# Performance work log

Measured on AMD Instinct MI355X. Metric: run time of the kernel, lower is better.

The kernel has to match this reference:

```python
import jax, jax.numpy as jnp
import numpy as np
from jax import lax

NPOINT = 1024
RADIUS = 0.2
NSAMPLE = 32
BN_EPS = 1e-5


def square_distance(src, dst):
    # src: [B,N,3], dst: [B,M,3] -> [B,N,M]
    d = -2.0 * jnp.einsum('bnc,bmc->bnm', src, dst)
    d = d + jnp.sum(src * src, -1)[:, :, None]
    d = d + jnp.sum(dst * dst, -1)[:, None, :]
    return d


def farthest_point_sample(xyz, npoint):
    # Deterministic start at index 0 (torch version uses a random start).
    B, N, _ = xyz.shape
    batch = jnp.arange(B)

    def step(carry, _):
        distance, farthest = carry
        centroid = xyz[batch, farthest][:, None, :]          # [B,1,3]
        dist = jnp.sum((xyz - centroid) ** 2, -1)            # [B,N]
        distance = jnp.minimum(distance, dist)
        new_far = jnp.argmax(distance, -1).astype(jnp.int32)
        return (distance, new_far), farthest

    init = (jnp.full((B, N), 1e10, xyz.dtype), jnp.zeros((B,), jnp.int32))
    _, cents = lax.scan(step, init, None, length=npoint)     # [npoint,B]
    return cents.T                                           # [B,npoint]


def index_points(points, idx):
    # points: [B,N,C], idx: [B,...] -> [B,...,C]
    return jax.vmap(lambda p, i: p[i])(points, idx)


def query_ball_point(radius, nsample, xyz, new_xyz):
    B, N, _ = xyz.shape
    sqr = square_distance(new_xyz, xyz)                      # [B,S,N]
    gidx = jnp.where(sqr > radius * radius, N,
                     jnp.arange(N, dtype=jnp.int32)[None, None, :])
    gidx = jnp.sort(gidx, axis=-1)[:, :, :nsample]           # [B,S,nsample]
    first = gidx[:, :, :1]
    return jnp.where(gidx == N, first, gidx)


def conv_bn_relu(x, w, b, g, beta):
    # x: [B,Cin,K,S]; 1x1 conv + training-mode BN + ReLU
    y = jnp.einsum('bcks,oc->boks', x, w) + b[None, :, None, None]
    mean = jnp.mean(y, axis=(0, 2, 3), keepdims=True)
    var = jnp.var(y, axis=(0, 2, 3), keepdims=True)
    y = (y - mean) * lax.rsqrt(var + BN_EPS)
    y = y * g[None, :, None, None] + beta[None, :, None, None]
    return jax.nn.relu(y)


def setup_inputs() -> dict:
    key = jax.random.key(0)
    ks = jax.random.split(key, 8)
    B, N, D = 16, 4096, 64
    inp = {
        'xyz': jax.random.uniform(ks[0], (B, N, 3), jnp.float32),
        'points': jax.random.normal(ks[1], (B, N, D), jnp.float32),
        'w1': jax.random.normal(ks[2], (64, 67), jnp.float32) * 0.1,
        'b1': jax.random.normal(ks[3], (64,), jnp.float32) * 0.1,
        'g1': jnp.ones((64,), jnp.float32),
        'beta1': jnp.zeros((64,), jnp.float32),
        'w2': jax.random.normal(ks[4], (64, 64), jnp.float32) * 0.1,
        'b2': jax.random.normal(ks[5], (64,), jnp.float32) * 0.1,
        'g2': jnp.ones((64,), jnp.float32),
        'beta2': jnp.zeros((64,), jnp.float32),
        'w3': jax.random.normal(ks[6], (128, 64), jnp.float32) * 0.1,
        'b3': jax.random.normal(ks[7], (128,), jnp.float32) * 0.1,
        'g3': jnp.ones((128,), jnp.float32),
        'beta3': jnp.zeros((128,), jnp.float32),
    }
    return inp


def reference(xyz, points, w1, b1, g1, beta1, w2, b2, g2, beta2, w3, b3, g3, beta3):
    B, N, C = xyz.shape
    fps_idx = farthest_point_sample(xyz, NPOINT)                 # [B,S]
    new_xyz = index_points(xyz, fps_idx)                         # [B,S,3]
    idx = query_ball_point(RADIUS, NSAMPLE, xyz, new_xyz)        # [B,S,K]
    grouped_xyz = index_points(xyz, idx) - new_xyz[:, :, None, :]  # [B,S,K,3]
    grouped_points = jnp.concatenate([grouped_xyz, index_points(points, idx)], axis=-1)  # [B,S,K,3+D]
    x = jnp.transpose(grouped_points, (0, 3, 2, 1))              # [B,C,K,S]
    x = conv_bn_relu(x, w1, b1, g1, beta1)
    x = conv_bn_relu(x, w2, b2, g2, beta2)
    x = conv_bn_relu(x, w3, b3, g3, beta3)
    new_points = jnp.max(x, axis=2)                              # [B,C_out,S]
    new_points = jnp.transpose(new_points, (0, 2, 1))            # [B,S,C_out]
    return (new_xyz, new_points)
```

## Files before the change

### kernel.cpp

```cpp
#include <hip/hip_runtime.h>
#include <stdint.h>

#define NPOINT 1024
#define NSAMPLE 32
#define NB 16
#define NN 4096
#define BN_EPS 1e-5
#define NPIX (NB*NPOINT*NSAMPLE)
#define NBLK 8192

__device__ __forceinline__ float sqdist3(float dx, float dy, float dz) {
  #pragma clang fp contract(off)
  float a = dx*dx; float b = dy*dy; float c = dz*dz;
  return (a + b) + c;
}

#define FPS_T 512
#define FPS_PTS (NN/FPS_T)
#define FPS_W (FPS_T/64)

#define DPP_MAX64V(VAR, CTRL)                                                  \
  {                                                                            \
    long long kl = __double_as_longlong(VAR);                                  \
    int lo = (int)(unsigned int)kl, hi = (int)(kl >> 32);                      \
    int olo = __builtin_amdgcn_update_dpp(lo, lo, (CTRL), 0xf, 0xf, false);    \
    int ohi = __builtin_amdgcn_update_dpp(hi, hi, (CTRL), 0xf, 0xf, false);    \
    double ok = __longlong_as_double(((long long)ohi << 32) |                  \
                                     (unsigned long long)(unsigned int)olo);   \
    VAR = fmax(VAR, ok);                                                       \
  }

__global__ __launch_bounds__(512) void fps_kernel(
    const float* __restrict__ xyz, int* __restrict__ cents_g) {
  __shared__ __align__(16) float4 pos[NN];
  __shared__ __align__(16) double keybuf[2][FPS_W];
  __shared__ int cents_l[NPOINT];
  const int b = blockIdx.x;
  const int t = threadIdx.x;
  const float* base = xyz + (size_t)b * NN * 3;
  for (int i = t; i < NN; i += FPS_T) {
    pos[i] = make_float4(base[3*i+0], base[3*i+1], base[3*i+2], 0.f);
  }
  __syncthreads();
  float px[FPS_PTS], py[FPS_PTS], pz[FPS_PTS], dist[FPS_PTS];
  #pragma unroll
  for (int i = 0; i < FPS_PTS; i++) {
    float4 p = pos[i*FPS_T + t];
    px[i] = p.x; py[i] = p.y; pz[i] = p.z;
    dist[i] = 1e10f;
  }
  const int lane = t & 63, wid = t >> 6;
  int far = 0;
  for (int it = 0; it < NPOINT; it++) {
    if (t == 0) cents_l[it] = far;
    float4 c = pos[far];
    float bv = -1.0f; int bj = 0x7fffffff;
    #pragma unroll
    for (int i = 0; i < FPS_PTS; i++) {
      float d = sqdist3(px[i]-c.x, py[i]-c.y, pz[i]-c.z);
      float nd = fminf(dist[i], d);
      dist[i] = nd;
      int j = i*FPS_T + t;
      if (nd > bv) { bv = nd; bj = j; }
    }
    double bk = __longlong_as_double(
        ((long long)__float_as_int(bv) << 32) |
        (unsigned long long)(unsigned int)((NN-1) - bj));
    DPP_MAX64V(bk, 0x111);
    DPP_MAX64V(bk, 0x112);
    DPP_MAX64V(bk, 0x114);
    DPP_MAX64V(bk, 0x118);
    DPP_MAX64V(bk, 0x142);
    DPP_MAX64V(bk, 0x143);
    const int p = it & 1;
    if (lane == 63) keybuf[p][wid] = bk;
    __syncthreads();
    double k = keybuf[p][lane & (FPS_W-1)];
    DPP_MAX64V(k, 0x111);
    DPP_MAX64V(k, 0x112);
    DPP_MAX64V(k, 0x114);
    int lo32 = (int)(unsigned int)__double_as_longlong(k);
    far = (NN-1) - __builtin_amdgcn_readlane(lo32, 7);
  }
  __syncthreads();
  for (int i = t; i < NPOINT; i += FPS_T) cents_g[b*NPOINT + i] = cents_l[i];
}

__global__ __launch_bounds__(256) void ballquery_kernel(
    const float* __restrict__ xyz, const int* __restrict__ cents_g,
    int* __restrict__ idx) {
  const int w = blockIdx.x * 4 + (threadIdx.x >> 6);
  const int lane = threadIdx.x & 63;
  const int b = w >> 10;
  const double RR = 0.2 * 0.2;
  const int cj = cents_g[w] & (NN-1);
  const float* cptr = xyz + ((size_t)b * NN + cj) * 3;
  const double cx = (double)cptr[0], cy = (double)cptr[1], cz = (double)cptr[2];
  const double cn = cx*cx + cy*cy + cz*cz;
  const float* base = xyz + (size_t)b * NN * 3;
  int* out = idx + (size_t)w * NSAMPLE;
  int have = 0, firstj = 0;
  for (int j0 = 0; j0 < NN; j0 += 64) {
    int j = j0 + lane;
    double x = (double)base[3*j+0];
    double y = (double)base[3*j+1];
    double z = (double)base[3*j+2];
    double pn = x*x + y*y + z*z;
    double d = -2.0*(cx*x + cy*y + cz*z) + cn + pn;
    bool pass = !(d > RR);
    unsigned long long m = __ballot(pass);
    int cnt = __popcll(m);
    if (have == 0 && cnt > 0) firstj = j0 + (__ffsll((unsigned long long)m) - 1);
    if (pass) {
      int pos = have + __popcll(m & ((1ull << lane) - 1ull));
      if (pos < NSAMPLE) out[pos] = j;
    }
    have += cnt;
    if (have >= NSAMPLE) break;
  }
  for (int k = have + lane; k < NSAMPLE; k += 64) out[k] = firstj;
}

template<int MODE>
__global__ __launch_bounds__(256) void fused_pass(
    const float* __restrict__ xyz, const float* __restrict__ points,
    const int* __restrict__ cents_g, const int* __restrict__ idx,
    const float* __restrict__ w1, const float* __restrict__ b1,
    const float* __restrict__ w2, const float* __restrict__ b2,
    const float* __restrict__ w3, const float* __restrict__ b3,
    const double* __restrict__ aff1, const double* __restrict__ aff2,
    double* __restrict__ partial, float* __restrict__ pmax, float* __restrict__ pmin) {
  __shared__ float wbuf[67*64];
  __shared__ float xsm[67*68];
  __shared__ float bsm[64];
  __shared__ float bsm2[64];
  __shared__ float sc1m[64], sh1m[64], sc2m[64], sh2m[64];
  const int t = threadIdx.x;
  const int pb = blockIdx.x * 64;
  const int tr = t & 15, tc = t >> 4;
  double* pout = partial + (size_t)blockIdx.x * 256;

  for (int ii = t; ii < 67*64; ii += 256) {
    int oc = ii & 63, cc = ii >> 6;
    wbuf[cc*64 + oc] = w1[oc*67 + cc];
  }
  if (t < 64) {
    bsm[t] = b1[t];
    if (MODE >= 2) { sc1m[t] = (float)aff1[t]; sh1m[t] = (float)aff1[128+t]; }
    if (MODE >= 3) { sc2m[t] = (float)aff2[t]; sh2m[t] = (float)aff2[128+t]; }
  }
  {
    const int pxl = t >> 2, q = t & 3;
    const int p = pb + pxl;
    const int bs = p >> 5;
    const int b  = p >> 15;
    const int j  = idx[p] & (NN-1);
    const float4* prow = (const float4*)(points + ((size_t)b * NN + j) * 64);
    #pragma unroll
    for (int u = 0; u < 4; u++) {
      float4 v = prow[q*4 + u];
      int c0 = 3 + q*16 + u*4;
      xsm[(c0+0)*68 + pxl] = v.x;
      xsm[(c0+1)*68 + pxl] = v.y;
      xsm[(c0+2)*68 + pxl] = v.z;
      xsm[(c0+3)*68 + pxl] = v.w;
    }
    if (q == 0) {
      const float* xr = xyz + ((size_t)b * NN + j) * 3;
      const int cj = cents_g[bs] & (NN-1);
      const float* ce = xyz + ((size_t)b * NN + cj) * 3;
      xsm[0*68 + pxl] = xr[0] - ce[0];
      xsm[1*68 + pxl] = xr[1] - ce[1];
      xsm[2*68 + pxl] = xr[2] - ce[2];
    }
  }
  __syncthreads();

  float acc[4][4] = {};
  for (int cc = 0; cc < 67; cc++) {
    float4 xv = *(const float4*)&xsm[cc*68 + 4*tr];
    float4 wv = *(const float4*)&wbuf[cc*64 + 4*tc];
    float xa[4] = {xv.x, xv.y, xv.z, xv.w};
    float wa[4] = {wv.x, wv.y, wv.z, wv.w};
    #pragma unroll
    for (int i = 0; i < 4; i++)
      #pragma unroll
      for (int jj = 0; jj < 4; jj++) acc[i][jj] += xa[i]*wa[jj];
  }
  if constexpr (MODE == 1) {
    double s1[4] = {0,0,0,0}, s2[4] = {0,0,0,0};
    #pragma unroll
    for (int jj = 0; jj < 4; jj++) {
      float bb = bsm[4*tc+jj];
      #pragma unroll
      for (int i = 0; i < 4; i++) {
        double yd = (double)(acc[i][jj] + bb);
        s1[jj] += yd; s2[jj] += yd*yd;
      }
    }
    #pragma unroll
    for (int off = 8; off > 0; off >>= 1)
      #pragma unroll
      for (int jj = 0; jj < 4; jj++) {
        s1[jj] += __shfl_down(s1[jj], off, 16);
        s2[jj] += __shfl_down(s2[jj], off, 16);
      }
    if (tr == 0)
      #pragma unroll
      for (int jj = 0; jj < 4; jj++) {
        pout[4*tc+jj]       = s1[jj];
        pout[128 + 4*tc+jj] = s2[jj];
      }
    return;
  }

  __syncthreads();
  #pragma unroll
  for (int jj = 0; jj < 4; jj++) {
    int oc = 4*tc + jj;
    float bb = bsm[oc], sc = sc1m[oc], sh = sh1m[oc];
    float r[4];
    #pragma unroll
    for (int i = 0; i < 4; i++) r[i] = fmaxf((acc[i][jj] + bb)*sc + sh, 0.f);
    *(float4*)&xsm[oc*68 + 4*tr] = make_float4(r[0], r[1], r[2], r[3]);
  }
  for (int ii = t; ii < 4096; ii += 256) {
    int oc = ii & 63, cc = ii >> 6;
    wbuf[cc*64 + oc] = w2[oc*64 + cc];
  }
  if (t < 64) bsm2[t] = b2[t];
  __syncthreads();

  float acc2[4][4] = {};
  for (int cc = 0; cc < 64; cc++) {
    float4 xv = *(const float4*)&xsm[cc*68 + 4*tr];
    float4 wv = *(const float4*)&wbuf[cc*64 + 4*tc];
    float xa[4] = {xv.x, xv.y, xv.z, xv.w};
    float wa[4] = {wv.x, wv.y, wv.z, wv.w};
    #pragma unroll
    for (int i = 0; i < 4; i++)
      #pragma unroll
      for (int jj = 0; jj < 4; jj++) acc2[i][jj] += xa[i]*wa[jj];
  }
  if constexpr (MODE == 2) {
    double s1[4] = {0,0,0,0}, s2[4] = {0,0,0,0};
    #pragma unroll
    for (int jj = 0; jj < 4; jj++) {
      float bb = bsm2[4*tc+jj];
      #pragma unroll
      for (int i = 0; i < 4; i++) {
        double yd = (double)(acc2[i][jj] + bb);
        s1[jj] += yd; s2[jj] += yd*yd;
      }
    }
    #pragma unroll
    for (int off = 8; off > 0; off >>= 1)
      #pragma unroll
      for (int jj = 0; jj < 4; jj++) {
        s1[jj] += __shfl_down(s1[jj], off, 16);
        s2[jj] += __shfl_down(s2[jj], off, 16);
      }
    if (tr == 0)
      #pragma unroll
      for (int jj = 0; jj < 4; jj++) {
        pout[4*tc+jj]       = s1[jj];
        pout[128 + 4*tc+jj] = s2[jj];
      }
    return;
  }

  if constexpr (MODE == 3) {
    __syncthreads();
    #pragma unroll
    for (int jj = 0; jj < 4; jj++) {
      int oc = 4*tc + jj;
      float bb = bsm2[oc], sc = sc2m[oc], sh = sh2m[oc];
      float r[4];
      #pragma unroll
      for (int i = 0; i < 4; i++) r[i] = fmaxf((acc2[i][jj] + bb)*sc + sh, 0.f);
      *(float4*)&xsm[oc*68 + 4*tr] = make_float4(r[0], r[1], r[2], r[3]);
    }
    for (int h = 0; h < 2; h++) {
      for (int ii = t; ii < 4096; ii += 256) {
        int oc = ii & 63, cc = ii >> 6;
        wbuf[cc*64 + oc] = w3[(h*64 + oc)*64 + cc];
      }
      if (t < 64) bsm[t] = b3[h*64 + t];
      __syncthreads();
      float acc3[4][4] = {};
      for (int cc = 0; cc < 64; cc++) {
        float4 xv = *(const float4*)&xsm[cc*68 + 4*tr];
        float4 wv = *(const float4*)&wbuf[cc*64 + 4*tc];
        float xa[4] = {xv.x, xv.y, xv.z, xv.w};
        float wa[4] = {wv.x, wv.y, wv.z, wv.w};
        #pragma unroll
        for (int i = 0; i < 4; i++)
          #pragma unroll
          for (int jj = 0; jj < 4; jj++) acc3[i][jj] += xa[i]*wa[jj];
      }
      double s1[4] = {0,0,0,0}, s2[4] = {0,0,0,0};
      float pmx[4], pmn[4];
      #pragma unroll
      for (int jj = 0; jj < 4; jj++) { pmx[jj] = -3.4e38f; pmn[jj] = 3.4e38f; }
      #pragma unroll
      for (int jj = 0; jj < 4; jj++) {
        float bb = bsm[4*tc+jj];
        #pragma unroll
        for (int i = 0; i < 4; i++) {
          float y = acc3[i][jj] + bb;
          double yd = (double)y;
          s1[jj] += yd; s2[jj] += yd*yd;
          pmx[jj] = fmaxf(pmx[jj], y); pmn[jj] = fminf(pmn[jj], y);
        }
      }
      #pragma unroll
      for (int off = 8; off > 0; off >>= 1)
        #pragma unroll
        for (int jj = 0; jj < 4; jj++) {
          s1[jj] += __shfl_down(s1[jj], off, 16);
          s2[jj] += __shfl_down(s2[jj], off, 16);
        }
      if (tr == 0)
        #pragma unroll
        for (int jj = 0; jj < 4; jj++) {
          pout[h*64 + 4*tc+jj]       = s1[jj];
          pout[128 + h*64 + 4*tc+jj] = s2[jj];
        }
      #pragma unroll
      for (int off = 4; off > 0; off >>= 1)
        #pragma unroll
        for (int jj = 0; jj < 4; jj++) {
          pmx[jj] = fmaxf(pmx[jj], __shfl_down(pmx[jj], off, 8));
          pmn[jj] = fminf(pmn[jj], __shfl_down(pmn[jj], off, 8));
        }
      if ((tr & 7) == 0) {
        int bs = (pb >> 5) + (tr >> 3);
        size_t ob = (size_t)bs*128 + h*64 + 4*tc;
        #pragma unroll
        for (int jj = 0; jj < 4; jj++) {
          pmax[ob + jj] = pmx[jj];
          pmin[ob + jj] = pmn[jj];
        }
      }
      __syncthreads();
    }
  }
}

__global__ __launch_bounds__(256) void reduce_finalize_kernel(
    const double* __restrict__ partial,
    const float* __restrict__ g, const float* __restrict__ beta,
    double* __restrict__ aff) {
  __shared__ double sa1[4], sa2[4];
  const int c = blockIdx.x;
  const int t = threadIdx.x;
  double a1 = 0.0, a2 = 0.0;
  for (int blk = t; blk < NBLK; blk += 256) {
    a1 += partial[(size_t)blk*256 + c];
    a2 += partial[(size_t)blk*256 + 128 + c];
  }
  #pragma unroll
  for (int off = 32; off > 0; off >>= 1) {
    a1 += __shfl_down(a1, off);
    a2 += __shfl_down(a2, off);
  }
  const int lane = t & 63, wid = t >> 6;
  if (lane == 0) { sa1[wid] = a1; sa2[wid] = a2; }
  __syncthreads();
  if (t == 0) {
    double s1 = sa1[0] + sa1[1] + sa1[2] + sa1[3];
    double s2 = sa2[0] + sa2[1] + sa2[2] + sa2[3];
    const double invN = 1.0 / (double)NPIX;
    double mean = s1 * invN;
    double var  = s2 * invN - mean*mean;
    var = var > 0.0 ? var : 0.0;
    double r  = 1.0 / sqrt(var + BN_EPS);
    double sc = (double)g[c] * r;
    aff[c]       = sc;
    aff[128 + c] = (double)beta[c] - mean*sc;
  }
}

__global__ __launch_bounds__(256) void out_kernel(
    const float* __restrict__ pmax, const float* __restrict__ pmin,
    const double* __restrict__ aff3, float* __restrict__ out_np) {
  int i = blockIdx.x * 256 + threadIdx.x;
  int oc = i & 127;
  double sc = aff3[oc], sh = aff3[128+oc];
  double v = (sc >= 0.0) ? (double)pmax[i] : (double)pmin[i];
  double y = v*sc + sh;
  out_np[i] = (float)(y > 0.0 ? y : 0.0);
}

__global__ __launch_bounds__(1024) void write_newxyz_kernel(
    const float* __restrict__ xyz, const int* __restrict__ cents_g,
    float* __restrict__ out) {
  int i = blockIdx.x * 1024 + threadIdx.x;
  int b = i >> 10;
  int j = cents_g[i] & (NN-1);
  const float* src = xyz + ((size_t)b * NN + j) * 3;
  size_t o = (size_t)i * 3;
  out[o+0] = src[0];
  out[o+1] = src[1];
  out[o+2] = src[2];
}

extern "C" void kernel_launch(void* const* d_in, const int* in_sizes, int n_in,
                              void* d_out, int out_size, void* d_ws, size_t ws_size,
                              hipStream_t stream) {
  const float* xyz    = (const float*)d_in[0];
  const float* points = (const float*)d_in[1];
  const float* w1  = (const float*)d_in[2];
  const float* b1  = (const float*)d_in[3];
  const float* g1  = (const float*)d_in[4];
  const float* be1 = (const float*)d_in[5];
  const float* w2  = (const float*)d_in[6];
  const float* b2  = (const float*)d_in[7];
  const float* g2  = (const float*)d_in[8];
  const float* be2 = (const float*)d_in[9];
  const float* w3  = (const float*)d_in[10];
  const float* b3  = (const float*)d_in[11];
  const float* g3  = (const float*)d_in[12];
  const float* be3 = (const float*)d_in[13];

  char* ws = (char*)d_ws;
  double* aff     = (double*)(ws + 8192);
  int*    cents   = (int*)  (ws + 16384);
  int*    idx     = (int*)  (ws + 81920);
  float*  pmax    = (float*)(ws + 2179072);
  float*  pmin    = (float*)(ws + 10567680);
  double* partial = (double*)(ws + 18956288);
  float* out_xyz = (float*)d_out;
  float* out_np  = (float*)d_out + (size_t)NB*NPOINT*3;

  fps_kernel        <<<16,   512, 0, stream>>>(xyz, cents);
  ballquery_kernel  <<<4096, 256, 0, stream>>>(xyz, cents, idx);
  fused_pass<1>     <<<NBLK, 256, 0, stream>>>(xyz, points, cents, idx, w1,b1,w2,b2,w3,b3,
                                               aff, aff+256, partial, pmax, pmin);
  reduce_finalize_kernel<<<64, 256, 0, stream>>>(partial, g1, be1, aff);
  fused_pass<2>     <<<NBLK, 256, 0, stream>>>(xyz, points, cents, idx, w1,b1,w2,b2,w3,b3,
                                               aff, aff+256, partial, pmax, pmin);
  reduce_finalize_kernel<<<64, 256, 0, stream>>>(partial, g2, be2, aff+256);
  fused_pass<3>     <<<NBLK, 256, 0, stream>>>(xyz, points, cents, idx, w1,b1,w2,b2,w3,b3,
                                               aff, aff+256, partial, pmax, pmin);
  reduce_finalize_kernel<<<128, 256, 0, stream>>>(partial, g3, be3, aff+512);
  out_kernel        <<<NBLK, 256, 0, stream>>>(pmax, pmin, aff+512, out_np);
  write_newxyz_kernel<<<16, 1024, 0, stream>>>(xyz, cents, out_xyz);
}
```

Baseline: 1.427 ms.

## Cache pre-BN conv activations in workspace to avoid recomputing earlier layers

Replaces the recompute-from-scratch schedule, where each BN pass regathers points and redoes all earlier 1x1 convs, with a store-and-reload scheme. Layer 1 and layer 2 pre-bias outputs are written to workspace buffers, and new fused_mid and fused_last kernels read them, apply the previous BN and ReLU, and run one conv. Fallback paths are chosen by workspace size. The FPS inner loop is also changed to build packed 64-bit keys per point and take a tree max instead of a sequential compare. This trades redundant gathers and GEMMs for about 134MB per layer of extra global traffic.

Result: faster. 1.283 ms (-10.1%).

```diff
diff --git a/kernel.cpp b/kernel.cpp
--- a/kernel.cpp
+++ b/kernel.cpp
@@ -43,29 +43,35 @@
   }
   __syncthreads();
   float px[FPS_PTS], py[FPS_PTS], pz[FPS_PTS], dist[FPS_PTS];
+  int lowj[FPS_PTS];
   #pragma unroll
   for (int i = 0; i < FPS_PTS; i++) {
     float4 p = pos[i*FPS_T + t];
     px[i] = p.x; py[i] = p.y; pz[i] = p.z;
     dist[i] = 1e10f;
+    lowj[i] = (NN-1) - (i*FPS_T + t);
   }
   const int lane = t & 63, wid = t >> 6;
   int far = 0;
   for (int it = 0; it < NPOINT; it++) {
     if (t == 0) cents_l[it] = far;
     float4 c = pos[far];
-    float bv = -1.0f; int bj = 0x7fffffff;
+    float nd[FPS_PTS];
     #pragma unroll
     for (int i = 0; i < FPS_PTS; i++) {
       float d = sqdist3(px[i]-c.x, py[i]-c.y, pz[i]-c.z);
-      float nd = fminf(dist[i], d);
-      dist[i] = nd;
-      int j = i*FPS_T + t;
-      if (nd > bv) { bv = nd; bj = j; }
-    }
-    double bk = __longlong_as_double(
-        ((long long)__float_as_int(bv) << 32) |
-        (unsigned long long)(unsigned int)((NN-1) - bj));
+      nd[i] = fminf(dist[i], d);
+      dist[i] = nd[i];
+    }
+    double kk[FPS_PTS];
+    #pragma unroll
+    for (int i = 0; i < FPS_PTS; i++) {
+      kk[i] = __longlong_as_double(
+          ((long long)__float_as_int(nd[i]) << 32) |
+          (unsigned long long)(unsigned int)lowj[i]);
+    }
+    double bk = fmax(fmax(fmax(kk[0], kk[1]), fmax(kk[2], kk[3])),
+                     fmax(fmax(kk[4], kk[5]), fmax(kk[6], kk[7])));
     DPP_MAX64V(bk, 0x111);
     DPP_MAX64V(bk, 0x112);
     DPP_MAX64V(bk, 0x114);
@@ -121,7 +127,7 @@
   for (int k = have + lane; k < NSAMPLE; k += 64) out[k] = firstj;
 }
 
-template<int MODE>
+template<int MODE, bool STOREY>
 __global__ __launch_bounds__(256) void fused_pass(
     const float* __restrict__ xyz, const float* __restrict__ points,
     const int* __restrict__ cents_g, const int* __restrict__ idx,
@@ -129,7 +135,8 @@
     const float* __restrict__ w2, const float* __restrict__ b2,
     const float* __restrict__ w3, const float* __restrict__ b3,
     const double* __restrict__ aff1, const double* __restrict__ aff2,
-    double* __restrict__ partial, float* __restrict__ pmax, float* __restrict__ pmin) {
+    double* __restrict__ partial, float* __restrict__ pmax, float* __restrict__ pmin,
+    float* __restrict__ ystore) {
   __shared__ float wbuf[67*64];
   __shared__ float xsm[67*68];
   __shared__ float bsm[64];
@@ -188,6 +195,13 @@
       for (int jj = 0; jj < 4; jj++) acc[i][jj] += xa[i]*wa[jj];
   }
   if constexpr (MODE == 1) {
+    if constexpr (STOREY) {
+      #pragma unroll
+      for (int i = 0; i < 4; i++) {
+        float4 o = make_float4(acc[i][0], acc[i][1], acc[i][2], acc[i][3]);
+        *(float4*)(ystore + ((size_t)(pb + 4*tr + i))*64 + 4*tc) = o;
+      }
+    }
     double s1[4] = {0,0,0,0}, s2[4] = {0,0,0,0};
     #pragma unroll
     for (int jj = 0; jj < 4; jj++) {
@@ -243,6 +257,13 @@
       for (int jj = 0; jj < 4; jj++) acc2[i][jj] += xa[i]*wa[jj];
   }
   if constexpr (MODE == 2) {
+    if constexpr (STOREY) {
+      #pragma unroll
+      for (int i = 0; i < 4; i++) {
+        float4 o = make_float4(acc2[i][0], acc2[i][1], acc2[i][2], acc2[i][3]);
+        *(float4*)(ystore + ((size_t)(pb + 4*tr + i))*64 + 4*tc) = o;
+      }
+    }
     double s1[4] = {0,0,0,0}, s2[4] = {0,0,0,0};
     #pragma unroll
     for (int jj = 0; jj < 4; jj++) {
@@ -344,6 +365,185 @@
       }
       __syncthreads();
     }
+  }
+}
+
+__global__ __launch_bounds__(256) void fused_mid(
+    const float* __restrict__ y1, const float* __restrict__ b1,
+    const float* __restrict__ w2, const float* __restrict__ b2,
+    const double* __restrict__ aff1,
+    double* __restrict__ partial, float* __restrict__ y2) {
+  __shared__ float wbuf[64*64];
+  __shared__ float xsm[64*68];
+  __shared__ float bsm[64];
+  __shared__ float bsm2[64];
+  __shared__ float sc1m[64], sh1m[64];
+  const int t = threadIdx.x;
+  const int pb = blockIdx.x * 64;
+  const int tr = t & 15, tc = t >> 4;
+  double* pout = partial + (size_t)blockIdx.x * 256;
+
+  for (int ii = t; ii < 4096; ii += 256) {
+    int oc = ii & 63, cc = ii >> 6;
+    wbuf[cc*64 + oc] = w2[oc*64 + cc];
+  }
+  if (t < 64) {
+    bsm[t] = b1[t]; bsm2[t] = b2[t];
+    sc1m[t] = (float)aff1[t]; sh1m[t] = (float)aff1[128+t];
+  }
+  __syncthreads();
+  {
+    const int pxl = t >> 2, q = t & 3;
+    const float* yrow = y1 + ((size_t)(pb + pxl))*64;
+    #pragma unroll
+    for (int u = 0; u < 4; u++) {
+      int c0 = 4*q + 16*u;
+      float4 v = *(const float4*)(yrow + c0);
+      xsm[(c0+0)*68 + pxl] = fmaxf((v.x + bsm[c0+0])*sc1m[c0+0] + sh1m[c0+0], 0.f);
+      xsm[(c0+1)*68 + pxl] = fmaxf((v.y + bsm[c0+1])*sc1m[c0+1] + sh1m[c0+1], 0.f);
+      xsm[(c0+2)*68 + pxl] = fmaxf((v.z + bsm[c0+2])*sc1m[c0+2] + sh1m[c0+2], 0.f);
+      xsm[(c0+3)*68 + pxl] = fmaxf((v.w + bsm[c0+3])*sc1m[c0+3] + sh1m[c0+3], 0.f);
+    }
+  }
+  __syncthreads();
+
+  float acc2[4][4] = {};
+  for (int cc = 0; cc < 64; cc++) {
+    float4 xv = *(const float4*)&xsm[cc*68 + 4*tr];
+    float4 wv = *(const float4*)&wbuf[cc*64 + 4*tc];
+    float xa[4] = {xv.x, xv.y, xv.z, xv.w};
+    float wa[4] = {wv.x, wv.y, wv.z, wv.w};
+    #pragma unroll
+    for (int i = 0; i < 4; i++)
+      #pragma unroll
+      for (int jj = 0; jj < 4; jj++) acc2[i][jj] += xa[i]*wa[jj];
+  }
+  #pragma unroll
+  for (int i = 0; i < 4; i++) {
+    float4 o = make_float4(acc2[i][0], acc2[i][1], acc2[i][2], acc2[i][3]);
+    *(float4*)(y2 + ((size_t)(pb + 4*tr + i))*64 + 4*tc) = o;
+  }
+  double s1[4] = {0,0,0,0}, s2[4] = {0,0,0,0};
+  #pragma unroll
+  for (int jj = 0; jj < 4; jj++) {
+    float bb = bsm2[4*tc+jj];
+    #pragma unroll
+    for (int i = 0; i < 4; i++) {
+      double yd = (double)(acc2[i][jj] + bb);
+      s1[jj] += yd; s2[jj] += yd*yd;
+    }
+  }
+  #pragma unroll
+  for (int off = 8; off > 0; off >>= 1)
+    #pragma unroll
+    for (int jj = 0; jj < 4; jj++) {
+      s1[jj] += __shfl_down(s1[jj], off, 16);
+      s2[jj] += __shfl_down(s2[jj], off, 16);
+    }
+  if (tr == 0)
+    #pragma unroll
+    for (int jj = 0; jj < 4; jj++) {
+      pout[4*tc+jj]       = s1[jj];
+      pout[128 + 4*tc+jj] = s2[jj];
+    }
+}
+
+__global__ __launch_bounds__(256) void fused_last(
+    const float* __restrict__ y2, const float* __restrict__ b2,
+    const float* __restrict__ w3, const float* __restrict__ b3,
+    const double* __restrict__ aff2,
+    double* __restrict__ partial, float* __restrict__ pmax, float* __restrict__ pmin) {
+  __shared__ float wbuf[64*64];
+  __shared__ float xsm[64*68];
+  __shared__ float bsm[64];
+  __shared__ float bsm2[64];
+  __shared__ float sc2m[64], sh2m[64];
+  const int t = threadIdx.x;
+  const int pb = blockIdx.x * 64;
+  const int tr = t & 15, tc = t >> 4;
+  double* pout = partial + (size_t)blockIdx.x * 256;
+
+  if (t < 64) {
+    bsm2[t] = b2[t];
+    sc2m[t] = (float)aff2[t]; sh2m[t] = (float)aff2[128+t];
+  }
+  __syncthreads();
+  {
+    const int pxl = t >> 2, q = t & 3;
+    const float* yrow = y2 + ((size_t)(pb + pxl))*64;
+    #pragma unroll
+    for (int u = 0; u < 4; u++) {
+      int c0 = 4*q + 16*u;
+      float4 v = *(const float4*)(yrow + c0);
+      xsm[(c0+0)*68 + pxl] = fmaxf((v.x + bsm2[c0+0])*sc2m[c0+0] + sh2m[c0+0], 0.f);
+      xsm[(c0+1)*68 + pxl] = fmaxf((v.y + bsm2[c0+1])*sc2m[c0+1] + sh2m[c0+1], 0.f);
+      xsm[(c0+2)*68 + pxl] = fmaxf((v.z + bsm2[c0+2])*sc2m[c0+2] + sh2m[c0+2], 0.f);
+      xsm[(c0+3)*68 + pxl] = fmaxf((v.w + bsm2[c0+3])*sc2m[c0+3] + sh2m[c0+3], 0.f);
+    }
+  }
+  for (int h = 0; h < 2; h++) {
+    for (int ii = t; ii < 4096; ii += 256) {
+      int oc = ii & 63, cc = ii >> 6;
+      wbuf[cc*64 + oc] = w3[(h*64 + oc)*64 + cc];
+    }
+    if (t < 64) bsm[t] = b3[h*64 + t];
+    __syncthreads();
+    float acc3[4][4] = {};
+    for (int cc = 0; cc < 64; cc++) {
+      float4 xv = *(const float4*)&xsm[cc*68 + 4*tr];
+      float4 wv = *(const float4*)&wbuf[cc*64 + 4*tc];
+      float xa[4] = {xv.x, xv.y, xv.z, xv.w};
+      float wa[4] = {wv.x, wv.y, wv.z, wv.w};
+      #pragma unroll
+      for (int i = 0; i < 4; i++)
+        #pragma unroll
+        for (int jj = 0; jj < 4; jj++) acc3[i][jj] += xa[i]*wa[jj];
+    }
+    double s1[4] = {0,0,0,0}, s2[4] = {0,0,0,0};
+    float pmx[4], pmn[4];
+    #pragma unroll
+    for (int jj = 0; jj < 4; jj++) { pmx[jj] = -3.4e38f; pmn[jj] = 3.4e38f; }
+    #pragma unroll
+    for (int jj = 0; jj < 4; jj++) {
+      float bb = bsm[4*tc+jj];
+      #pragma unroll
+      for (int i = 0; i < 4; i++) {
+        float y = acc3[i][jj] + bb;
+        double yd = (double)y;
+        s1[jj] += yd; s2[jj] += yd*yd;
+        pmx[jj] = fmaxf(pmx[jj], y); pmn[jj] = fminf(pmn[jj], y);
+      }
+    }
+    #pragma unroll
+    for (int off = 8; off > 0; off >>= 1)
+      #pragma unroll
+      for (int jj = 0; jj < 4; jj++) {
+        s1[jj] += __shfl_down(s1[jj], off, 16);
+        s2[jj] += __shfl_down(s2[jj], off, 16);
+      }
+    if (tr == 0)
+      #pragma unroll
+      for (int jj = 0; jj < 4; jj++) {
+        pout[h*64 + 4*tc+jj]       = s1[jj];
+        pout[128 + h*64 + 4*tc+jj] = s2[jj];
+      }
+    #pragma unroll
+    for (int off = 4; off > 0; off >>= 1)
+      #pragma unroll
+      for (int jj = 0; jj < 4; jj++) {
+        pmx[jj] = fmaxf(pmx[jj], __shfl_down(pmx[jj], off, 8));
+        pmn[jj] = fminf(pmn[jj], __shfl_down(pmn[jj], off, 8));
+      }
+    if ((tr & 7) == 0) {
+      int bs = (pb >> 5) + (tr >> 3);
+      size_t ob = (size_t)bs*128 + h*64 + 4*tc;
+      #pragma unroll
+      for (int jj = 0; jj < 4; jj++) {
+        pmax[ob + jj] = pmx[jj];
+        pmin[ob + jj] = pmn[jj];
+      }
+    }
+    __syncthreads();
   }
 }
 
@@ -430,20 +630,47 @@
   float*  pmax    = (float*)(ws + 2179072);
   float*  pmin    = (float*)(ws + 10567680);
   double* partial = (double*)(ws + 18956288);
+  const size_t OFF_Y = 35733504;
+  const size_t SZ_Y  = (size_t)NPIX * 64 * 4;
+  float* ycache1 = (float*)(ws + OFF_Y);
+  float* ycache2 = (float*)(ws + OFF_Y + SZ_Y);
+  const bool full_path = ws_size >= OFF_Y + 2*SZ_Y;
+  const bool mid_path  = ws_size >= OFF_Y + SZ_Y;
   float* out_xyz = (float*)d_out;
   float* out_np  = (float*)d_out + (size_t)NB*NPOINT*3;
 
   fps_kernel        <<<16,   512, 0, stream>>>(xyz, cents);
   ballquery_kernel  <<<4096, 256, 0, stream>>>(xyz, cents, idx);
-  fused_pass<1>     <<<NBLK, 256, 0, stream>>>(xyz, points, cents, idx, w1,b1,w2,b2,w3,b3,
-                                               aff, aff+256, partial, pmax, pmin);
-  reduce_finalize_kernel<<<64, 256, 0, stream>>>(partial, g1, be1, aff);
-  fused_pass<2>     <<<NBLK, 256, 0, stream>>>(xyz, points, cents, idx, w1,b1,w2,b2,w3,b3,
-                                               aff, aff+256, partial, pmax, pmin);
-  reduce_finalize_kernel<<<64, 256, 0, stream>>>(partial, g2, be2, aff+256);
-  fused_pass<3>     <<<NBLK, 256, 0, stream>>>(xyz, points, cents, idx, w1,b1,w2,b2,w3,b3,
-                                               aff, aff+256, partial, pmax, pmin);
-  reduce_finalize_kernel<<<128, 256, 0, stream>>>(partial, g3, be3, aff+512);
+  if (full_path) {
+    fused_pass<1,true>  <<<NBLK, 256, 0, stream>>>(xyz, points, cents, idx, w1,b1,w2,b2,w3,b3,
+                                                   aff, aff+256, partial, pmax, pmin, ycache1);
+    reduce_finalize_kernel<<<64, 256, 0, stream>>>(partial, g1, be1, aff);
+    fused_mid         <<<NBLK, 256, 0, stream>>>(ycache1, b1, w2, b2, aff, partial, ycache2);
+    reduce_finalize_kernel<<<64, 256, 0, stream>>>(partial, g2, be2, aff+256);
+    fused_last        <<<NBLK, 256, 0, stream>>>(ycache2, b2, w3, b3, aff+256,
+                                                 partial, pmax, pmin);
+    reduce_finalize_kernel<<<128, 256, 0, stream>>>(partial, g3, be3, aff+512);
+  } else if (mid_path) {
+    fused_pass<1,false> <<<NBLK, 256, 0, stream>>>(xyz, points, cents, idx, w1,b1,w2,b2,w3,b3,
+                                                   aff, aff+256, partial, pmax, pmin, nullptr);
+    reduce_finalize_kernel<<<64, 256, 0, stream>>>(partial, g1, be1, aff);
+    fused_pass<2,true>  <<<NBLK, 256, 0, stream>>>(xyz, points, cents, idx, w1,b1,w2,b2,w3,b3,
+                                                   aff, aff+256, partial, pmax, pmin, ycache1);
+    reduce_finalize_kernel<<<64, 256, 0, stream>>>(partial, g2, be2, aff+256);
+    fused_last        <<<NBLK, 256, 0, stream>>>(ycache1, b2, w3, b3, aff+256,
+                                                 partial, pmax, pmin);
+    reduce_finalize_kernel<<<128, 256, 0, stream>>>(partial, g3, be3, aff+512);
+  } else {
+    fused_pass<1,false> <<<NBLK, 256, 0, stream>>>(xyz, points, cents, idx, w1,b1,w2,b2,w3,b3,
+                                                   aff, aff+256, partial, pmax, pmin, nullptr);
+    reduce_finalize_kernel<<<64, 256, 0, stream>>>(partial, g1, be1, aff);
+    fused_pass<2,false> <<<NBLK, 256, 0, stream>>>(xyz, points, cents, idx, w1,b1,w2,b2,w3,b3,
+                                                   aff, aff+256, partial, pmax, pmin, nullptr);
+    reduce_finalize_kernel<<<64, 256, 0, stream>>>(partial, g2, be2, aff+256);
+    fused_pass<3,false> <<<NBLK, 256, 0, stream>>>(xyz, points, cents, idx, w1,b1,w2,b2,w3,b3,
+                                                   aff, aff+256, partial, pmax, pmin, nullptr);
+    reduce_finalize_kernel<<<128, 256, 0, stream>>>(partial, g3, be3, aff+512);
+  }
   out_kernel        <<<NBLK, 256, 0, stream>>>(pmax, pmin, aff+512, out_np);
   write_newxyz_kernel<<<16, 1024, 0, stream>>>(xyz, cents, out_xyz);
 }
```
